# Optimization experiments

Measured on AMD Instinct MI355X. Metric: run time of the kernel, lower is better.

Reference implementation:

```python
import jax, jax.numpy as jnp
import numpy as np


def setup_inputs() -> dict:
    key = jax.random.key(0)
    k1, k2, k3, k4 = jax.random.split(key, 4)
    B, T, H = 4, 512, 256
    scale = 1.0 / np.sqrt(H)
    return {
        "rnn_outputs": jax.random.normal(k1, (B, T, H), dtype=jnp.float32),
        "W1": jax.random.normal(k2, (H, H), dtype=jnp.float32) * scale,
        "W2": jax.random.normal(k3, (H, H), dtype=jnp.float32) * scale,
        "v": jax.random.normal(k4, (H,), dtype=jnp.float32) * scale,
    }


def reference(rnn_outputs, W1, W2, v):
    """Bahdanau additive self-attention with causal mask.

    rnn_outputs: (B, T, H). Returns (context (B,T,H), weights (B,T,T)).
    """
    B, T, H = rnn_outputs.shape
    # nn.Linear applies x @ W.T
    query = rnn_outputs @ W1.T            # (B, T, H)
    keys = rnn_outputs @ W2.T             # (B, T, H)
    # scores[b,t,s] = v . tanh(q[b,t] + k[b,s]); materializes (B,T,T,H) like the original
    scores = jnp.einsum(
        "btsh,h->bts", jnp.tanh(query[:, :, None, :] + keys[:, None, :, :]), v
    )
    causal = jnp.triu(jnp.ones((T, T), dtype=bool), k=1)  # mask future positions
    scores = jnp.where(causal[None], -jnp.inf, scores)
    weights = jax.nn.softmax(scores, axis=-1)
    weights = jnp.nan_to_num(weights)
    context = jnp.einsum("bts,bsh->bth", weights, rnn_outputs)
    return context, weights
```

## Files before the change

### kernel.cpp

```cpp
#include <hip/hip_runtime.h>

namespace {

constexpr int kB = 4;
constexpr int kT = 512;
constexpr int kH = 256;

__device__ __forceinline__ float rcpf(float x) {
  return __builtin_amdgcn_rcpf(x);
}

__global__ __launch_bounds__(256) void transpose_w_kernel(
    const float* __restrict__ W1, const float* __restrict__ W2,
    float* __restrict__ Wt1, float* __restrict__ Wt2) {
  __shared__ float tile[32][33];
  const float* Win = (blockIdx.z == 0) ? W1 : W2;
  float* Wout = (blockIdx.z == 0) ? Wt1 : Wt2;
  const int jo = blockIdx.x * 32, ho = blockIdx.y * 32;
  const int c = threadIdx.x & 31, r0 = threadIdx.x >> 5;
#pragma unroll
  for (int p = 0; p < 4; ++p)
    tile[r0 + 8 * p][c] = Win[(size_t)(ho + r0 + 8 * p) * kH + jo + c];
  __syncthreads();
#pragma unroll
  for (int p = 0; p < 4; ++p)
    Wout[(size_t)(jo + r0 + 8 * p) * kH + ho + c] = tile[c][r0 + 8 * p];
}

__global__ __launch_bounds__(256) void proj_kernel(
    const float* __restrict__ X, const float* __restrict__ Wt1,
    const float* __restrict__ Wt2, float* __restrict__ EQt,
    float* __restrict__ EKt) {
  __shared__ __align__(16) float ws4[4][16][kH];

  const int tid = threadIdx.x;
  const int w = tid >> 6, lane = tid & 63;
  const int row0 = blockIdx.x * 8;
  const float* Wt = (blockIdx.y == 0) ? Wt1 : Wt2;
  float* dst = (blockIdx.y == 0) ? EQt : EKt;

  const float* gw = Wt + (size_t)(4 * w) * kH + lane * 4;

#define PSTAGE(buf, c)                                                       \
  {                                                                          \
    const size_t go = (size_t)(c) * 16 * kH;                                 \
    __builtin_amdgcn_global_load_lds(                                        \
        (const __attribute__((address_space(1))) void*)(gw + go),            \
        (__attribute__((address_space(3))) void*)&ws4[buf][4 * w][0], 16, 0, \
        0);                                                                  \
    __builtin_amdgcn_global_load_lds(                                        \
        (const __attribute__((address_space(1))) void*)(gw + go + kH),       \
        (__attribute__((address_space(3))) void*)&ws4[buf][4 * w + 1][0], 16,\
        0, 0);                                                               \
    __builtin_amdgcn_global_load_lds(                                        \
        (const __attribute__((address_space(1))) void*)(gw + go + 2 * kH),   \
        (__attribute__((address_space(3))) void*)&ws4[buf][4 * w + 2][0], 16,\
        0, 0);                                                               \
    __builtin_amdgcn_global_load_lds(                                        \
        (const __attribute__((address_space(1))) void*)(gw + go + 3 * kH),   \
        (__attribute__((address_space(3))) void*)&ws4[buf][4 * w + 3][0], 16,\
        0, 0);                                                               \
  }

  float acc[8];
#pragma unroll
  for (int i = 0; i < 8; ++i) acc[i] = 0.0f;

  PSTAGE(0, 0)
  PSTAGE(1, 1)
  PSTAGE(2, 2)

#pragma unroll 1
  for (int c = 0; c < 16; ++c) {
    if (c <= 13) {
      asm volatile("s_waitcnt vmcnt(8)" ::: "memory");
    } else if (c == 14) {
      asm volatile("s_waitcnt vmcnt(4)" ::: "memory");
    } else {
      asm volatile("s_waitcnt vmcnt(0)" ::: "memory");
    }
    __builtin_amdgcn_s_barrier();
    __builtin_amdgcn_sched_barrier(0);
    if (c <= 12) PSTAGE((c + 3) & 3, c + 3)
    const int bf = c & 3;
#pragma unroll
    for (int u = 0; u < 16; ++u) {
      const float wv = ws4[bf][u][tid];
#pragma unroll
      for (int i = 0; i < 8; ++i)
        acc[i] = __builtin_fmaf(X[(size_t)(row0 + i) * kH + c * 16 + u], wv,
                                acc[i]);
    }
  }
#undef PSTAGE

  const int bb = row0 >> 9, r0 = row0 & (kT - 1);
  float* out = dst + ((size_t)(bb * kH + tid)) * kT + r0;
  float4 lo = {__expf(2.0f * acc[0]), __expf(2.0f * acc[1]),
               __expf(2.0f * acc[2]), __expf(2.0f * acc[3])};
  float4 hi = {__expf(2.0f * acc[4]), __expf(2.0f * acc[5]),
               __expf(2.0f * acc[6]), __expf(2.0f * acc[7])};
  *reinterpret_cast<float4*>(out) = lo;
  *reinterpret_cast<float4*>(out + 4) = hi;
}

__global__ __launch_bounds__(256) void score_kernel(
    const float* __restrict__ EQt, const float* __restrict__ EKt,
    const float* __restrict__ v, float* __restrict__ Sc) {
  __shared__ __align__(16) float eqs[4][32 * 32];
  __shared__ __align__(16) float eks[4][32 * 32];

  const int tid = threadIdx.x;
  const int w = tid >> 6, lane = tid & 63;
  const int blk = blockIdx.x;
  const int xcd = blk & 7;
  const int b = xcd >> 1;
  const int tIdx = (xcd & 1) * 68 + (blk >> 3);

  int ti = (int)((__builtin_sqrtf(8.0f * (float)tIdx + 1.0f) - 1.0f) * 0.5f);
  while ((ti + 1) * (ti + 2) / 2 <= tIdx) ++ti;
  while (ti * (ti + 1) / 2 > tIdx) --ti;
  const int si = tIdx - ti * (ti + 1) / 2;
  const int t0 = ti * 32, s0 = si * 32;

  const int hoff = w * 8 + (lane >> 3);
  const int coff = (lane & 7) * 4;
  const float* gq = EQt + ((size_t)(b * kH + hoff) * kT) + t0 + coff;
  const float* gk = EKt + ((size_t)(b * kH + hoff) * kT) + s0 + coff;
  float* lqw = &eqs[0][0] + w * 256;
  float* lkw = &eks[0][0] + w * 256;

#define STAGE(buf, c)                                                        \
  {                                                                          \
    const size_t go = (size_t)(c) * 32 * kT;                                 \
    __builtin_amdgcn_global_load_lds(                                        \
        (const __attribute__((address_space(1))) void*)(gq + go),            \
        (__attribute__((address_space(3))) void*)(lqw + (buf)*1024), 16, 0,  \
        0);                                                                  \
    __builtin_amdgcn_global_load_lds(                                        \
        (const __attribute__((address_space(1))) void*)(gk + go),            \
        (__attribute__((address_space(3))) void*)(lkw + (buf)*1024), 16, 0,  \
        0);                                                                  \
  }

  const int wt = w >> 1, wsx = w & 1;
  const int tq = wt * 16 + 2 * (lane >> 3);
  const int sk = wsx * 16 + 2 * (lane & 7);

  float ac0 = 0.f, ac1 = 0.f, ac2 = 0.f, ac3 = 0.f;
  float ac4 = 0.f, ac5 = 0.f, ac6 = 0.f, ac7 = 0.f;

  STAGE(0, 0)
  STAGE(1, 1)
  STAGE(2, 2)

#pragma unroll 1
  for (int c = 0; c < 8; ++c) {
    if (c <= 5) {
      asm volatile("s_waitcnt vmcnt(4)" ::: "memory");
    } else if (c == 6) {
      asm volatile("s_waitcnt vmcnt(2)" ::: "memory");
    } else {
      asm volatile("s_waitcnt vmcnt(0)" ::: "memory");
    }
    __builtin_amdgcn_s_barrier();
    __builtin_amdgcn_sched_barrier(0);
    if (c <= 4) STAGE((c + 3) & 3, c + 3)
    const int boff = (c & 3) * 1024;
    const float* vp = v + c * 32;
#pragma unroll
    for (int h = 0; h < 32; h += 2) {
      const float2 qA = *reinterpret_cast<const float2*>(&eqs[0][boff + h * 32 + tq]);
      const float2 kA = *reinterpret_cast<const float2*>(&eks[0][boff + h * 32 + sk]);
      const float2 qB = *reinterpret_cast<const float2*>(&eqs[0][boff + h * 32 + 32 + tq]);
      const float2 kB = *reinterpret_cast<const float2*>(&eks[0][boff + h * 32 + 32 + sk]);
      const float vA = vp[h], vB = vp[h + 1];
      ac0 = __builtin_fmaf(vA, rcpf(__builtin_fmaf(qA.x, kA.x, 1.0f)), ac0);
      ac1 = __builtin_fmaf(vA, rcpf(__builtin_fmaf(qA.x, kA.y, 1.0f)), ac1);
      ac2 = __builtin_fmaf(vA, rcpf(__builtin_fmaf(qA.y, kA.x, 1.0f)), ac2);
      ac3 = __builtin_fmaf(vA, rcpf(__builtin_fmaf(qA.y, kA.y, 1.0f)), ac3);
      ac4 = __builtin_fmaf(vB, rcpf(__builtin_fmaf(qB.x, kB.x, 1.0f)), ac4);
      ac5 = __builtin_fmaf(vB, rcpf(__builtin_fmaf(qB.x, kB.y, 1.0f)), ac5);
      ac6 = __builtin_fmaf(vB, rcpf(__builtin_fmaf(qB.y, kB.x, 1.0f)), ac6);
      ac7 = __builtin_fmaf(vB, rcpf(__builtin_fmaf(qB.y, kB.y, 1.0f)), ac7);
    }
  }
#undef STAGE

  float vv = v[lane] + v[lane + 64] + v[lane + 128] + v[lane + 192];
#pragma unroll
  for (int off = 32; off > 0; off >>= 1) vv += __shfl_xor(vv, off, 64);

  float2 row0v = {__builtin_fmaf(-2.0f, ac0 + ac4, vv),
                  __builtin_fmaf(-2.0f, ac1 + ac5, vv)};
  float2 row1v = {__builtin_fmaf(-2.0f, ac2 + ac6, vv),
                  __builtin_fmaf(-2.0f, ac3 + ac7, vv)};
  float* so = Sc + ((size_t)(b * kT + t0 + tq)) * kT + s0 + sk;
  *reinterpret_cast<float2*>(so) = row0v;
  *reinterpret_cast<float2*>(so + kT) = row1v;
}

__global__ __launch_bounds__(512) void attn2_kernel(
    const float* __restrict__ X, float* wsc, float* __restrict__ ctx) {
  __shared__ float wls[8][kT + 8];
  __shared__ float pc[2][8][kH];

  const int id = blockIdx.x;
  const int xcd = id & 7;
  const int b = xcd >> 1;
  const int sub = (xcd & 1) * 32 + (id >> 3);
  const int row0 = sub * 8;
  const int tid = threadIdx.x;
  const int w = tid >> 6, lane = tid & 63;

  const int t = row0 + w;
  float* srow = wsc + ((size_t)(b * kT + t)) * kT;
  const int sbase8 = lane * 8;
  float4 s4a = *reinterpret_cast<const float4*>(srow + sbase8);
  float4 s4b = *reinterpret_cast<const float4*>(srow + sbase8 + 4);
  float p[8];
  p[0] = (sbase8 + 0 <= t) ? __expf(s4a.x) : 0.f;
  p[1] = (sbase8 + 1 <= t) ? __expf(s4a.y) : 0.f;
  p[2] = (sbase8 + 2 <= t) ? __expf(s4a.z) : 0.f;
  p[3] = (sbase8 + 3 <= t) ? __expf(s4a.w) : 0.f;
  p[4] = (sbase8 + 4 <= t) ? __expf(s4b.x) : 0.f;
  p[5] = (sbase8 + 5 <= t) ? __expf(s4b.y) : 0.f;
  p[6] = (sbase8 + 6 <= t) ? __expf(s4b.z) : 0.f;
  p[7] = (sbase8 + 7 <= t) ? __expf(s4b.w) : 0.f;
  float l = ((p[0] + p[1]) + (p[2] + p[3])) + ((p[4] + p[5]) + (p[6] + p[7]));
#pragma unroll
  for (int off = 32; off > 0; off >>= 1) l += __shfl_xor(l, off, 64);
  const float rs = rcpf(l);
#pragma unroll
  for (int j = 0; j < 8; ++j) p[j] *= rs;
  float4 o4a = {p[0], p[1], p[2], p[3]};
  float4 o4b = {p[4], p[5], p[6], p[7]};
  *reinterpret_cast<float4*>(srow + sbase8) = o4a;
  *reinterpret_cast<float4*>(srow + sbase8 + 4) = o4b;
#pragma unroll
  for (int j = 0; j < 8; ++j) wls[w][sbase8 + j] = p[j];
  __syncthreads();

  const int h = tid & (kH - 1);
  const int half = tid >> 8;
  const float* Xb = X + ((size_t)b * kT) * kH + h;
  float acc[8];
#pragma unroll
  for (int r = 0; r < 8; ++r) acc[r] = 0.f;
  const int sb = half * 256;
#pragma unroll 2
  for (int so = 0; so < 256; so += 4) {
    const int s = sb + so;
    const float x0 = Xb[(size_t)(s + 0) * kH];
    const float x1 = Xb[(size_t)(s + 1) * kH];
    const float x2 = Xb[(size_t)(s + 2) * kH];
    const float x3 = Xb[(size_t)(s + 3) * kH];
#pragma unroll
    for (int r = 0; r < 8; ++r) {
      const float4 wr = *reinterpret_cast<const float4*>(&wls[r][s]);
      float a = __builtin_fmaf(wr.x, x0, acc[r]);
      a = __builtin_fmaf(wr.y, x1, a);
      a = __builtin_fmaf(wr.z, x2, a);
      acc[r] = __builtin_fmaf(wr.w, x3, a);
    }
  }
#pragma unroll
  for (int r = 0; r < 8; ++r) pc[half][r][h] = acc[r];
  __syncthreads();

#pragma unroll
  for (int q = 0; q < 4; ++q) {
    const int idx = q * 512 + tid;
    const int r = idx >> 8, hh = idx & (kH - 1);
    ctx[((size_t)(b * kT + row0 + r)) * kH + hh] = pc[0][r][hh] + pc[1][r][hh];
  }
}

}

extern "C" void kernel_launch(void* const* d_in, const int* in_sizes, int n_in,
                              void* d_out, int out_size, void* d_ws,
                              size_t ws_size, hipStream_t stream) {
  const float* X = (const float*)d_in[0];
  const float* W1 = (const float*)d_in[1];
  const float* W2 = (const float*)d_in[2];
  const float* v = (const float*)d_in[3];

  float* ctx = (float*)d_out;
  float* wout = ctx + (size_t)kB * kT * kH;
  float* Wt1 = wout;
  float* Wt2 = wout + (size_t)kH * kH;
  float* Sc = wout;
  float* EQt = (float*)d_ws;
  float* EKt = EQt + (size_t)kB * kH * kT;

  transpose_w_kernel<<<dim3(8, 8, 2), 256, 0, stream>>>(W1, W2, Wt1, Wt2);
  proj_kernel<<<dim3(kB * kT / 8, 2), 256, 0, stream>>>(X, Wt1, Wt2, EQt, EKt);
  score_kernel<<<544, 256, 0, stream>>>(EQt, EKt, v, Sc);
  attn2_kernel<<<256, 512, 0, stream>>>(X, Sc, ctx);
}
```

Measured before the change: 66.44 us.

## Pair reciprocals in score loop and vectorize context reduction across waves

In the score kernel, each pair of terms vA/dA + vB/dB is merged into one fraction (vB*dA + vA*dB)/(dA*dB). This halves the number of quarter-rate reciprocal instructions at the cost of an extra multiply and FMA, and it drops four accumulators. The context kernel is reorganized so each lane handles four contiguous h values with float4 loads of X, and each wave covers its own 64-position slice of s. Partial sums are then reduced through a larger LDS buffer. The trade-off is more LDS use and a possible precision or overflow risk in the product dA*dB.

```diff
diff --git a/kernel.cpp b/kernel.cpp
--- a/kernel.cpp
+++ b/kernel.cpp
@@ -148,7 +148,6 @@
   const int sk = wsx * 16 + 2 * (lane & 7);
 
   float ac0 = 0.f, ac1 = 0.f, ac2 = 0.f, ac3 = 0.f;
-  float ac4 = 0.f, ac5 = 0.f, ac6 = 0.f, ac7 = 0.f;
 
   STAGE(0, 0)
   STAGE(1, 1)
@@ -175,14 +174,30 @@
       const float2 qB = *reinterpret_cast<const float2*>(&eqs[0][boff + h * 32 + 32 + tq]);
       const float2 kB = *reinterpret_cast<const float2*>(&eks[0][boff + h * 32 + 32 + sk]);
       const float vA = vp[h], vB = vp[h + 1];
-      ac0 = __builtin_fmaf(vA, rcpf(__builtin_fmaf(qA.x, kA.x, 1.0f)), ac0);
-      ac1 = __builtin_fmaf(vA, rcpf(__builtin_fmaf(qA.x, kA.y, 1.0f)), ac1);
-      ac2 = __builtin_fmaf(vA, rcpf(__builtin_fmaf(qA.y, kA.x, 1.0f)), ac2);
-      ac3 = __builtin_fmaf(vA, rcpf(__builtin_fmaf(qA.y, kA.y, 1.0f)), ac3);
-      ac4 = __builtin_fmaf(vB, rcpf(__builtin_fmaf(qB.x, kB.x, 1.0f)), ac4);
-      ac5 = __builtin_fmaf(vB, rcpf(__builtin_fmaf(qB.x, kB.y, 1.0f)), ac5);
-      ac6 = __builtin_fmaf(vB, rcpf(__builtin_fmaf(qB.y, kB.x, 1.0f)), ac6);
-      ac7 = __builtin_fmaf(vB, rcpf(__builtin_fmaf(qB.y, kB.y, 1.0f)), ac7);
+      {
+        const float dA = __builtin_fmaf(qA.x, kA.x, 1.0f);
+        const float dB = __builtin_fmaf(qB.x, kB.x, 1.0f);
+        const float nm = __builtin_fmaf(vB, dA, vA * dB);
+        ac0 = __builtin_fmaf(nm, rcpf(dA * dB), ac0);
+      }
+      {
+        const float dA = __builtin_fmaf(qA.x, kA.y, 1.0f);
+        const float dB = __builtin_fmaf(qB.x, kB.y, 1.0f);
+        const float nm = __builtin_fmaf(vB, dA, vA * dB);
+        ac1 = __builtin_fmaf(nm, rcpf(dA * dB), ac1);
+      }
+      {
+        const float dA = __builtin_fmaf(qA.y, kA.x, 1.0f);
+        const float dB = __builtin_fmaf(qB.y, kB.x, 1.0f);
+        const float nm = __builtin_fmaf(vB, dA, vA * dB);
+        ac2 = __builtin_fmaf(nm, rcpf(dA * dB), ac2);
+      }
+      {
+        const float dA = __builtin_fmaf(qA.y, kA.y, 1.0f);
+        const float dB = __builtin_fmaf(qB.y, kB.y, 1.0f);
+        const float nm = __builtin_fmaf(vB, dA, vA * dB);
+        ac3 = __builtin_fmaf(nm, rcpf(dA * dB), ac3);
+      }
     }
   }
 #undef STAGE
@@ -191,10 +206,10 @@
 #pragma unroll
   for (int off = 32; off > 0; off >>= 1) vv += __shfl_xor(vv, off, 64);
 
-  float2 row0v = {__builtin_fmaf(-2.0f, ac0 + ac4, vv),
-                  __builtin_fmaf(-2.0f, ac1 + ac5, vv)};
-  float2 row1v = {__builtin_fmaf(-2.0f, ac2 + ac6, vv),
-                  __builtin_fmaf(-2.0f, ac3 + ac7, vv)};
+  float2 row0v = {__builtin_fmaf(-2.0f, ac0, vv),
+                  __builtin_fmaf(-2.0f, ac1, vv)};
+  float2 row1v = {__builtin_fmaf(-2.0f, ac2, vv),
+                  __builtin_fmaf(-2.0f, ac3, vv)};
   float* so = Sc + ((size_t)(b * kT + t0 + tq)) * kT + s0 + sk;
   *reinterpret_cast<float2*>(so) = row0v;
   *reinterpret_cast<float2*>(so + kT) = row1v;
@@ -203,7 +218,7 @@
 __global__ __launch_bounds__(512) void attn2_kernel(
     const float* __restrict__ X, float* wsc, float* __restrict__ ctx) {
   __shared__ float wls[8][kT + 8];
-  __shared__ float pc[2][8][kH];
+  __shared__ __align__(16) float pc[8][8][kH];
 
   const int id = blockIdx.x;
   const int xcd = id & 7;
@@ -241,39 +256,58 @@
   for (int j = 0; j < 8; ++j) wls[w][sbase8 + j] = p[j];
   __syncthreads();
 
-  const int h = tid & (kH - 1);
-  const int half = tid >> 8;
-  const float* Xb = X + ((size_t)b * kT) * kH + h;
-  float acc[8];
-#pragma unroll
-  for (int r = 0; r < 8; ++r) acc[r] = 0.f;
-  const int sb = half * 256;
+  const int h4 = lane * 4;
+  const float* Xb = X + ((size_t)b * kT) * kH + h4;
+  float4 acc4[8];
+#pragma unroll
+  for (int r = 0; r < 8; ++r) acc4[r] = {0.f, 0.f, 0.f, 0.f};
+
 #pragma unroll 2
-  for (int so = 0; so < 256; so += 4) {
-    const int s = sb + so;
-    const float x0 = Xb[(size_t)(s + 0) * kH];
-    const float x1 = Xb[(size_t)(s + 1) * kH];
-    const float x2 = Xb[(size_t)(s + 2) * kH];
-    const float x3 = Xb[(size_t)(s + 3) * kH];
+  for (int so = 0; so < 64; so += 4) {
+    const int s = (w << 6) + so;
+    const float4 x0 = *reinterpret_cast<const float4*>(Xb + (size_t)(s + 0) * kH);
+    const float4 x1 = *reinterpret_cast<const float4*>(Xb + (size_t)(s + 1) * kH);
+    const float4 x2 = *reinterpret_cast<const float4*>(Xb + (size_t)(s + 2) * kH);
+    const float4 x3 = *reinterpret_cast<const float4*>(Xb + (size_t)(s + 3) * kH);
 #pragma unroll
     for (int r = 0; r < 8; ++r) {
       const float4 wr = *reinterpret_cast<const float4*>(&wls[r][s]);
-      float a = __builtin_fmaf(wr.x, x0, acc[r]);
-      a = __builtin_fmaf(wr.y, x1, a);
-      a = __builtin_fmaf(wr.z, x2, a);
-      acc[r] = __builtin_fmaf(wr.w, x3, a);
-    }
-  }
-#pragma unroll
-  for (int r = 0; r < 8; ++r) pc[half][r][h] = acc[r];
+      float4 a = acc4[r];
+      a.x = __builtin_fmaf(wr.x, x0.x, a.x);
+      a.y = __builtin_fmaf(wr.x, x0.y, a.y);
+      a.z = __builtin_fmaf(wr.x, x0.z, a.z);
+      a.w = __builtin_fmaf(wr.x, x0.w, a.w);
+      a.x = __builtin_fmaf(wr.y, x1.x, a.x);
+      a.y = __builtin_fmaf(wr.y, x1.y, a.y);
+      a.z = __builtin_fmaf(wr.y, x1.z, a.z);
+      a.w = __builtin_fmaf(wr.y, x1.w, a.w);
+      a.x = __builtin_fmaf(wr.z, x2.x, a.x);
+      a.y = __builtin_fmaf(wr.z, x2.y, a.y);
+      a.z = __builtin_fmaf(wr.z, x2.z, a.z);
+      a.w = __builtin_fmaf(wr.z, x2.w, a.w);
+      a.x = __builtin_fmaf(wr.w, x3.x, a.x);
+      a.y = __builtin_fmaf(wr.w, x3.y, a.y);
+      a.z = __builtin_fmaf(wr.w, x3.z, a.z);
+      a.w = __builtin_fmaf(wr.w, x3.w, a.w);
+      acc4[r] = a;
+    }
+  }
+#pragma unroll
+  for (int r = 0; r < 8; ++r)
+    *reinterpret_cast<float4*>(&pc[w][r][h4]) = acc4[r];
   __syncthreads();
 
-#pragma unroll
-  for (int q = 0; q < 4; ++q) {
-    const int idx = q * 512 + tid;
-    const int r = idx >> 8, hh = idx & (kH - 1);
-    ctx[((size_t)(b * kT + row0 + r)) * kH + hh] = pc[0][r][hh] + pc[1][r][hh];
-  }
+  float4 sum = {0.f, 0.f, 0.f, 0.f};
+#pragma unroll
+  for (int c = 0; c < 8; ++c) {
+    const float4 q = *reinterpret_cast<const float4*>(&pc[c][w][h4]);
+    sum.x += q.x;
+    sum.y += q.y;
+    sum.z += q.z;
+    sum.w += q.w;
+  }
+  *reinterpret_cast<float4*>(
+      ctx + ((size_t)(b * kT + row0 + w)) * kH + h4) = sum;
 }
 
 }
```

After: 60.69 us (median of 2 runs). 1.09x faster.
